# Kernel optimization log

Hardware: AMD Instinct MI355X
Metric: run time of the kernel (lower is better)

Reference implementation:

```python
import jax, jax.numpy as jnp
import numpy as np

N_HEADS = 16
EPS = 1e-4


def setup_inputs() -> dict:
    key = jax.random.key(0)
    ks = jax.random.split(key, 9)
    B, L, E = 4, 4096, 1024
    s = 1.0 / np.sqrt(E)
    return {
        "x": jax.random.normal(ks[0], (B, L, E), dtype=jnp.float32),
        "Wq": jax.random.normal(ks[1], (E, E), dtype=jnp.float32) * s,
        "bq": jax.random.normal(ks[2], (E,), dtype=jnp.float32) * 0.01,
        "Wk": jax.random.normal(ks[3], (E, E), dtype=jnp.float32) * s,
        "bk": jax.random.normal(ks[4], (E,), dtype=jnp.float32) * 0.01,
        "Wv": jax.random.normal(ks[5], (E, E), dtype=jnp.float32) * s,
        "bv": jax.random.normal(ks[6], (E,), dtype=jnp.float32) * 0.01,
        "Wo": jax.random.normal(ks[7], (E, E), dtype=jnp.float32) * s,
        "bo": jax.random.normal(ks[8], (E,), dtype=jnp.float32) * 0.01,
    }


def _cosformer(x, Wq, bq, Wk, bk, Wv, bv, Wo, bo):
    B, L, E = x.shape
    H = N_HEADS
    hd = E // H
    # torch Linear: y = x @ W.T + b; self-attention so q=k=v source is x
    q = jax.nn.relu(jnp.einsum('ble,fe->blf', x, Wq) + bq)
    k = jax.nn.relu(jnp.einsum('ble,fe->blf', x, Wk) + bk)
    v = jnp.einsum('ble,fe->blf', x, Wv) + bv
    # (B, L, E) -> (B*H, L, hd)  [matches torch view(L, B*H, hd).transpose(0,1)]
    def split_heads(t):
        return t.reshape(B, L, H, hd).transpose(0, 2, 1, 3).reshape(B * H, L, hd)
    q, k, v = split_heads(q), split_heads(k), split_heads(v)
    m = L  # src_len == tgt_len
    idx = (np.pi / 2) * jnp.arange(1, m + 1, dtype=jnp.float32) / m  # (m,)
    sin = jnp.sin(idx)[None, :, None]
    cos = jnp.cos(idx)[None, :, None]
    q_ = jnp.concatenate([q * sin, q * cos], axis=-1)  # (BH, L, 2hd)
    k_ = jnp.concatenate([k * sin, k * cos], axis=-1)
    kv = jnp.einsum('nld,nlm->ndm', k_, v)             # (BH, 2hd, hd)
    z = 1.0 / jnp.maximum(jnp.einsum('nld,nd->nl', q_, k_.sum(axis=1)), EPS)
    attn = jnp.einsum('nld,ndm->nlm', q_, kv) * z[:, :, None]  # (BH, L, hd)
    # (B*H, L, hd) -> (B, L, E)
    out = attn.reshape(B, H, L, hd).transpose(0, 2, 1, 3).reshape(B, L, E)
    return jnp.einsum('ble,fe->blf', out, Wo) + bo


def reference(x, Wq, bq, Wk, bk, Wv, bv, Wo, bo):
    return _cosformer(x, Wq, bq, Wk, bk, Wv, bv, Wo, bo)
```

## Files before the change

kernel.cpp:

```cpp
#include <hip/hip_runtime.h>


typedef unsigned short u16;
typedef unsigned int u32;
typedef __attribute__((ext_vector_type(8))) __bf16 bf16x8;
typedef __attribute__((ext_vector_type(4))) float f32x4;

#define PI_HALF 1.57079632679489662f
#define EPS_Z 1e-4f

__device__ __forceinline__ u16 f32_to_bf16(float f) {
    union { float f; unsigned int u; } x; x.f = f;
    unsigned int lsb = (x.u >> 16) & 1u;
    x.u += 0x7fffu + lsb;
    return (u16)(x.u >> 16);
}
__device__ __forceinline__ float bf16_to_f32(u16 u) {
    union { float f; unsigned int u; } x; x.u = ((unsigned int)u) << 16;
    return x.f;
}

typedef __attribute__((address_space(1))) void amdgpu_global_t;
typedef __attribute__((address_space(3))) void amdgpu_lds_t;
__device__ __forceinline__ void async_load16(const u16* g, u16* l) {
    __builtin_amdgcn_global_load_lds((amdgpu_global_t*)g, (amdgpu_lds_t*)l, 16, 0, 0);
}

__global__ __launch_bounds__(256) void cvt_bf16(const float* __restrict__ in,
                                                u16* __restrict__ out, int n4) {
    int i = blockIdx.x * 256 + threadIdx.x;
    if (i >= n4) return;
    float4 f = ((const float4*)in)[i];
    ushort4 o;
    o.x = f32_to_bf16(f.x); o.y = f32_to_bf16(f.y);
    o.z = f32_to_bf16(f.z); o.w = f32_to_bf16(f.w);
    ((ushort4*)out)[i] = o;
}

__global__ __launch_bounds__(256) void cvt_w4(const float* __restrict__ w0,
                                              const float* __restrict__ w1,
                                              const float* __restrict__ w2,
                                              const float* __restrict__ w3,
                                              u16* __restrict__ wcat) {
    const float* src = (blockIdx.y == 0) ? w0 : (blockIdx.y == 1) ? w1
                     : (blockIdx.y == 2) ? w2 : w3;
    u16* dst = wcat + (size_t)blockIdx.y * 1048576;
    int i = blockIdx.x * 256 + threadIdx.x;
    float4 f = ((const float4*)src)[i];
    ushort4 o;
    o.x = f32_to_bf16(f.x); o.y = f32_to_bf16(f.y);
    o.z = f32_to_bf16(f.z); o.w = f32_to_bf16(f.w);
    ((ushort4*)dst)[i] = o;
}

__device__ __forceinline__ void gemm256_core(const u16* __restrict__ Abase,
                                             const u16* __restrict__ Bbase,
                                             u16* As, u16* Bs,
                                             f32x4 (&acc)[8][4]) {
    const int tid  = threadIdx.x;
    const int wave = tid >> 6;
    const int lane = tid & 63;
    const int quad = lane >> 4;
    const int l15  = lane & 15;
    const int wr   = wave >> 2;
    const int wc   = wave & 3;
    const int srow = tid >> 3;
    const int scg  = (tid & 7) ^ (srow & 7);

    const u16* Ag = Abase + ((long)srow << 10) + scg * 8;
    const u16* Bg = Bbase + ((long)srow << 10) + scg * 8;

    auto stage = [&](const u16* g, u16* lb, int hs, int t) {
        async_load16(g + ((long)hs << 16) + (t << 6), lb + hs * 4096);
    };
    auto rdA = [&](const u16* buf, int mf, int kk) -> bf16x8 {
        const int R = wr * 128 + mf * 16 + l15;
        return *(const bf16x8*)(buf + R * 64 + ((kk * 32 + quad * 8) ^ ((R & 7) * 8)));
    };
    auto rdB = [&](const u16* buf, int nf, int kk) -> bf16x8 {
        const int R = wc * 64 + nf * 16 + l15;
        return *(const bf16x8*)(buf + R * 64 + ((kk * 32 + quad * 8) ^ ((R & 7) * 8)));
    };

    bf16x8 a[4][2], b[4][2];
    auto mfma8 = [&](int i0, int j0) {
        __builtin_amdgcn_s_setprio(1);
#pragma unroll
        for (int i = 0; i < 4; ++i)
#pragma unroll
            for (int j = 0; j < 2; ++j)
#pragma unroll
                for (int kk = 0; kk < 2; ++kk)
                    acc[i0 + i][j0 + j] = __builtin_amdgcn_mfma_f32_16x16x32_bf16(
                        a[i][kk], b[j0 + j][kk], acc[i0 + i][j0 + j], 0, 0, 0);
        __builtin_amdgcn_s_setprio(0);
    };

#pragma unroll
    for (int hs = 0; hs < 4; ++hs) stage(Ag, As + wave * 512, hs, 0);
#pragma unroll
    for (int hs = 0; hs < 4; ++hs) stage(Bg, Bs + wave * 512, hs, 0);
#pragma unroll
    for (int hs = 0; hs < 4; ++hs) stage(Ag, As + 16384 + wave * 512, hs, 1);
#pragma unroll
    for (int hs = 0; hs < 4; ++hs) stage(Bg, Bs + 16384 + wave * 512, hs, 1);
    asm volatile("s_waitcnt vmcnt(8)" ::: "memory");
    __builtin_amdgcn_s_barrier();

#pragma unroll 1
    for (int t = 0; t < 16; ++t) {
        const int cur = t & 1;
        const u16* Ab = As + cur * 16384;
        const u16* Bb = Bs + cur * 16384;
        u16* lA = As + cur * 16384 + wave * 512;
        u16* lB = Bs + cur * 16384 + wave * 512;
        const bool pf = (t < 14);

#pragma unroll
        for (int i = 0; i < 4; ++i) { a[i][0] = rdA(Ab, i, 0); a[i][1] = rdA(Ab, i, 1); }
#pragma unroll
        for (int j = 0; j < 2; ++j) { b[j][0] = rdB(Bb, j, 0); b[j][1] = rdB(Bb, j, 1); }
        mfma8(0, 0);
#pragma unroll
        for (int j = 2; j < 4; ++j) { b[j][0] = rdB(Bb, j, 0); b[j][1] = rdB(Bb, j, 1); }
        mfma8(0, 2);
#pragma unroll
        for (int i = 0; i < 4; ++i) { a[i][0] = rdA(Ab, i + 4, 0); a[i][1] = rdA(Ab, i + 4, 1); }
        mfma8(4, 0);

        __builtin_amdgcn_s_barrier();
        asm volatile("" ::: "memory");
        if (pf) {
#pragma unroll
            for (int hs = 0; hs < 4; ++hs) stage(Bg, lB, hs, t + 2);
#pragma unroll
            for (int hs = 0; hs < 4; ++hs) stage(Ag, lA, hs, t + 2);
        }
        mfma8(4, 2);
        if (pf) {
            asm volatile("s_waitcnt vmcnt(8)" ::: "memory");
        } else {
            asm volatile("s_waitcnt vmcnt(0)" ::: "memory");
        }
        __builtin_amdgcn_s_barrier();
        asm volatile("" ::: "memory");
    }
}

__global__ __launch_bounds__(512, 2) void gemm_qkv(const u16* __restrict__ A,
                                                   const u16* __restrict__ Wcat,
                                                   const float* __restrict__ bq,
                                                   const float* __restrict__ bk,
                                                   const float* __restrict__ bv,
                                                   u16* __restrict__ qo,
                                                   u16* __restrict__ ko,
                                                   u16* __restrict__ vo) {
    __shared__ __align__(16) u16 As[32768];
    __shared__ __align__(16) u16 Bs[32768];
    const int bid = blockIdx.x;
    const int swz = (bid & 7) * 96 + (bid >> 3);
    const int bx  = swz / 12;
    const int byy = swz - bx * 12;
    const long tileM = (long)bx * 256;

    f32x4 acc[8][4] = {};
    gemm256_core(A + (tileM << 10), Wcat + ((long)byy << 18), As, Bs, acc);

    const int tid  = (int)threadIdx.x;
    const int wave = tid >> 6;
    const int lane = tid & 63;
    const int quad = lane >> 4, l15 = lane & 15;
    const int wr = wave >> 2, wc = wave & 3;
    const int mat = byy >> 2;
    const float* bias = (mat == 0) ? bq : (mat == 1) ? bk : bv;
    u16* outp = (mat == 0) ? qo : (mat == 1) ? ko : vo;
    const bool relu = (mat < 2);
    const int ncol0 = (byy & 3) * 256;

    const int rloc = tid >> 5;
    const int c8   = (tid & 31) * 8;
#pragma unroll 1
    for (int pass = 0; pass < 2; ++pass) {
        __syncthreads();
        if (wr == pass) {
#pragma unroll
            for (int i = 0; i < 8; ++i)
#pragma unroll
                for (int j = 0; j < 4; ++j) {
                    const int col = wc * 64 + j * 16 + l15;
                    const float bb = bias[ncol0 + col];
#pragma unroll
                    for (int r = 0; r < 4; ++r) {
                        const int row = i * 16 + quad * 4 + r;
                        float v = acc[i][j][r] + bb;
                        if (relu) v = fmaxf(v, 0.0f);
                        As[row * 256 + col] = f32_to_bf16(v);
                    }
                }
        }
        __syncthreads();
        const long gr0 = tileM + pass * 128;
#pragma unroll
        for (int it = 0; it < 8; ++it) {
            const int row = it * 16 + rloc;
            uint4 t4 = *(const uint4*)&As[row * 256 + c8];
            *(uint4*)&outp[(gr0 + row) * 1024 + ncol0 + c8] = t4;
        }
    }
}

__global__ __launch_bounds__(512, 2) void gemm_o(const u16* __restrict__ A,
                                                 const u16* __restrict__ Bw,
                                                 const float* __restrict__ bias,
                                                 float* __restrict__ Cout) {
    __shared__ __align__(16) u16 As[32768];
    __shared__ __align__(16) u16 Bs[32768];
    const int bid = blockIdx.x;
    const int swz = (bid & 7) * 32 + (bid >> 3);
    const long tileM = (long)(swz >> 2) * 256;
    const long tileN = (long)(swz & 3) * 256;

    f32x4 acc[8][4] = {};
    gemm256_core(A + (tileM << 10), Bw + (tileN << 10), As, Bs, acc);

    const int wave = (int)threadIdx.x >> 6;
    const int lane = (int)threadIdx.x & 63;
    const int quad = lane >> 4, l15 = lane & 15;
    const int wr = wave >> 2, wc = wave & 3;
#pragma unroll
    for (int j = 0; j < 4; ++j) {
        const long n = tileN + wc * 64 + j * 16 + l15;
        const float bb = bias[n];
#pragma unroll
        for (int i = 0; i < 8; ++i) {
            const long m0 = tileM + wr * 128 + i * 16 + quad * 4;
#pragma unroll
            for (int r = 0; r < 4; ++r)
                Cout[(m0 + r) * 1024 + n] = acc[i][j][r] + bb;
        }
    }
}

__global__ __launch_bounds__(256) void kv_mfma(const u16* __restrict__ kmat,
                                               const u16* __restrict__ vmat,
                                               float* __restrict__ part) {
    __shared__ u16 Ak[64 * 40];
    __shared__ u16 Bv[64 * 40];
    const int tid = threadIdx.x;
    const int wave = tid >> 6, lane = tid & 63;
    const int quad = lane >> 4, l15 = lane & 15;
    const int head = blockIdx.y;
    const int b = head >> 4, h = head & 15;
    const int l0 = blockIdx.x * 512;
    const int sl = tid >> 3;
    const int sc8 = tid & 7;
    const int scol = sl ^ ((sc8 & 3) << 3);
    const int krow_base = (wave & 1) * 32;
    const bool use_cos = (wave >> 1) != 0;
    const int mbase = wave * 32;

    float sv[8], cv[8];
#pragma unroll
    for (int e = 0; e < 8; e++) {
        float ang = (PI_HALF / 4096.0f) * (float)(l0 + quad * 8 + e + 1);
        sv[e] = sinf(ang); cv[e] = cosf(ang);
    }
    const float cD = 0.9999247018391445f;
    const float sD = 0.0122715382857199f;

    bf16x8 onesf;
#pragma unroll
    for (int e = 0; e < 8; e++)
        onesf[e] = (l15 == 0) ? (__bf16)1.0f : (__bf16)0.0f;

    f32x4 acc[2][5] = {};

    long row = ((long)b * 4096 + l0 + sl) * 1024 + h * 64 + sc8 * 8;
    uint4 kk = *(const uint4*)(kmat + row);
    uint4 vv = *(const uint4*)(vmat + row);

    for (int kt = 0; kt < 16; kt++) {
        uint4 kk_n = {}, vv_n = {};
        if (kt < 15) {
            row += 32 * 1024;
            kk_n = *(const uint4*)(kmat + row);
            vv_n = *(const uint4*)(vmat + row);
        }
        const u16* kp = (const u16*)&kk;
        const u16* vp = (const u16*)&vv;
#pragma unroll
        for (int e = 0; e < 8; e++) {
            const int d = sc8 * 8 + e;
            Ak[d * 40 + scol] = kp[e];
            Bv[d * 40 + scol] = vp[e];
        }
        __syncthreads();

        bf16x8 af[2];
#pragma unroll
        for (int i = 0; i < 2; i++) {
            const int d = krow_base + i * 16 + l15;
            const int q2 = (quad ^ ((d >> 3) & 3)) * 8;
            bf16x8 raw = *(const bf16x8*)&Ak[d * 40 + q2];
            bf16x8 sc;
#pragma unroll
            for (int e = 0; e < 8; e++)
                sc[e] = (__bf16)((float)raw[e] * (use_cos ? cv[e] : sv[e]));
            af[i] = sc;
        }
        bf16x8 bfr[5];
#pragma unroll
        for (int j = 0; j < 4; j++) {
            const int n = j * 16 + l15;
            const int q2 = (quad ^ ((n >> 3) & 3)) * 8;
            bfr[j] = *(const bf16x8*)&Bv[n * 40 + q2];
        }
        bfr[4] = onesf;
#pragma unroll
        for (int i = 0; i < 2; i++)
#pragma unroll
            for (int j = 0; j < 5; j++)
                acc[i][j] = __builtin_amdgcn_mfma_f32_16x16x32_bf16(
                    af[i], bfr[j], acc[i][j], 0, 0, 0);

#pragma unroll
        for (int e = 0; e < 8; e++) {
            const float ns = sv[e] * cD + cv[e] * sD;
            cv[e] = cv[e] * cD - sv[e] * sD;
            sv[e] = ns;
        }
        __syncthreads();
        kk = kk_n; vv = vv_n;
    }

    float* op = part + ((long)blockIdx.x * 64 + head) * 10240;
#pragma unroll
    for (int i = 0; i < 2; i++)
#pragma unroll
        for (int j = 0; j < 5; j++)
#pragma unroll
            for (int r = 0; r < 4; r++)
                op[(mbase + i * 16 + quad * 4 + r) * 80 + j * 16 + l15] = acc[i][j][r];
}

__global__ __launch_bounds__(256) void kv_reduce_t(const float* __restrict__ part,
                                                   u16* __restrict__ Bt) {
    __shared__ float accs[32 * 81];
    const int head = blockIdx.y, d2t = blockIdx.x;
    const float* bp = part + (long)head * 10240 + d2t * 32 * 80;
    for (int idx = threadIdx.x; idx < 2560; idx += 256) {
        float s = 0.0f;
#pragma unroll
        for (int c = 0; c < 8; c++) s += bp[(long)c * 655360 + idx];
        const int d2 = idx / 80, n = idx - d2 * 80;
        accs[d2 * 81 + n] = s;
    }
    __syncthreads();
    for (int idx = threadIdx.x; idx < 2560; idx += 256) {
        const int n = idx >> 5, d2 = idx & 31;
        Bt[(long)head * 10240 + n * 128 + d2t * 32 + d2] = f32_to_bf16(accs[d2 * 81 + n]);
    }
}

__global__ __launch_bounds__(256) void attn_mfma(const u16* __restrict__ qb,
                                                 const u16* __restrict__ Bt,
                                                 u16* __restrict__ merged) {
    __shared__ __align__(16) u16 As[128 * 72];
    __shared__ __align__(16) u16 Bs[80 * 136];
    const int tid = threadIdx.x;
    const int wave = tid >> 6, lane = tid & 63;
    const int quad = lane >> 4, l15 = lane & 15;
    const int head = blockIdx.y;
    const int b = head >> 4, h = head & 15;
    const int tm = blockIdx.x * 128;
    const long b4 = (long)b * 4096;

    for (int c = tid; c < 1024; c += 256) {
        const int row = c >> 3, c8 = c & 7;
        uint4 t = *(const uint4*)(qb + (b4 + tm + row) * 1024 + h * 64 + c8 * 8);
        *(uint4*)&As[row * 72 + c8 * 8] = t;
    }
    for (int c = tid; c < 1280; c += 256) {
        const int row = c >> 4, c16 = c & 15;
        uint4 t = *(const uint4*)(Bt + (long)head * 10240 + row * 128 + c16 * 8);
        *(uint4*)&Bs[row * 136 + c16 * 8] = t;
    }
    const int wm = wave * 32;
    float snl[2], csl[2];
#pragma unroll
    for (int i = 0; i < 2; i++) {
        const int l = tm + wm + i * 16 + l15;
        const float idx = PI_HALF * (float)(l + 1) * (1.0f / 4096.0f);
        snl[i] = sinf(idx); csl[i] = cosf(idx);
    }
    __syncthreads();

    f32x4 acc[2][5] = {};
#pragma unroll
    for (int kb = 0; kb < 4; kb++) {
        const int qc = (kb & 1) * 32 + quad * 8;
        bf16x8 af[2];
#pragma unroll
        for (int i = 0; i < 2; i++) {
            bf16x8 raw = *(const bf16x8*)&As[(wm + i * 16 + l15) * 72 + qc];
            const float s = (kb < 2) ? snl[i] : csl[i];
            bf16x8 sc;
#pragma unroll
            for (int e = 0; e < 8; e++) sc[e] = (__bf16)((float)raw[e] * s);
            af[i] = sc;
        }
        bf16x8 bf[5];
#pragma unroll
        for (int j = 0; j < 5; j++)
            bf[j] = *(const bf16x8*)&Bs[(j * 16 + l15) * 136 + kb * 32 + quad * 8];
#pragma unroll
        for (int i = 0; i < 2; i++)
#pragma unroll
            for (int j = 0; j < 5; j++)
                acc[i][j] = __builtin_amdgcn_mfma_f32_16x16x32_bf16(
                    af[i], bf[j], acc[i][j], 0, 0, 0);
    }

    __syncthreads();
#pragma unroll
    for (int i = 0; i < 2; i++) {
        float z[4];
#pragma unroll
        for (int r = 0; r < 4; r++) {
            const float den = __shfl(acc[i][4][r], lane & 0x30, 64);
            z[r] = 1.0f / fmaxf(den, EPS_Z);
        }
#pragma unroll
        for (int j = 0; j < 4; j++)
#pragma unroll
            for (int r = 0; r < 4; r++) {
                const int row = wm + i * 16 + quad * 4 + r;
                As[row * 64 + j * 16 + l15] = f32_to_bf16(acc[i][j][r] * z[r]);
            }
    }
    __syncthreads();
    const int rloc = tid >> 3, c8 = (tid & 7) * 8;
#pragma unroll
    for (int it = 0; it < 4; ++it) {
        const int row = it * 32 + rloc;
        uint4 t4 = *(const uint4*)&As[row * 64 + c8];
        *(uint4*)&merged[(b4 + tm + row) * 1024 + h * 64 + c8] = t4;
    }
}

extern "C" void kernel_launch(void* const* d_in, const int* in_sizes, int n_in,
                              void* d_out, int out_size, void* d_ws, size_t ws_size,
                              hipStream_t stream) {
    (void)in_sizes; (void)n_in; (void)out_size; (void)ws_size;
    const float* x  = (const float*)d_in[0];
    const float* Wq = (const float*)d_in[1];
    const float* bq = (const float*)d_in[2];
    const float* Wk = (const float*)d_in[3];
    const float* bk = (const float*)d_in[4];
    const float* Wv = (const float*)d_in[5];
    const float* bv = (const float*)d_in[6];
    const float* Wo = (const float*)d_in[7];
    const float* bo = (const float*)d_in[8];
    float* out = (float*)d_out;

    const int M = 16384, E = 1024;
    char* ws = (char*)d_ws;
    const size_t MB = 1048576;
    u16* xb   = (u16*)(ws);
    u16* qb   = (u16*)(ws + 32 * MB);
    u16* kb   = (u16*)(ws + 64 * MB);
    u16* vb   = (u16*)(ws + 96 * MB);
    u16* wcat = (u16*)(ws + 128 * MB);
    u16* wob  = wcat + 3 * (size_t)E * E;
    u16* Btb  = (u16*)(ws + 136 * MB);
    float* part = (float*)xb;
    u16* mergedb = kb;

    cvt_bf16<<<dim3(M * E / 4 / 256), dim3(256), 0, stream>>>(x, xb, M * E / 4);
    cvt_w4<<<dim3(E * E / 4 / 256, 4), dim3(256), 0, stream>>>(Wq, Wk, Wv, Wo, wcat);

    gemm_qkv<<<dim3(768), dim3(512), 0, stream>>>(xb, wcat, bq, bk, bv, qb, kb, vb);

    kv_mfma<<<dim3(8, 64), dim3(256), 0, stream>>>(kb, vb, part);
    kv_reduce_t<<<dim3(4, 64), dim3(256), 0, stream>>>(part, Btb);
    attn_mfma<<<dim3(32, 64), dim3(256), 0, stream>>>(qb, Btb, mergedb);

    gemm_o<<<dim3(256), dim3(512), 0, stream>>>(mergedb, wob, bo, out);
}
```

Measured before the change: 343.9 us.

## Shrink GEMM tiles to 128x256 with BK=32 for higher occupancy

Changes the shared GEMM core from 256x256 tiles with a K-step of 64 to 128x256 tiles with a K-step of 32. Shared memory per block drops from 128KB to 48KB and launch bounds rise to 4 blocks per CU. Both the QKV and output projection grids double to fill the CUs and hide latency. The LDS swizzle and the epilogue staging layout are redone to match. In exchange, each tile reuses its data less, so more global and LDS traffic per FLOP, and the loop runs more barrier iterations.

```diff
diff --git a/kernel.cpp b/kernel.cpp
--- a/kernel.cpp
+++ b/kernel.cpp
@@ -14,10 +14,6 @@
     unsigned int lsb = (x.u >> 16) & 1u;
     x.u += 0x7fffu + lsb;
     return (u16)(x.u >> 16);
-}
-__device__ __forceinline__ float bf16_to_f32(u16 u) {
-    union { float f; unsigned int u; } x; x.u = ((unsigned int)u) << 16;
-    return x.f;
 }
 
 typedef __attribute__((address_space(1))) void amdgpu_global_t;
@@ -53,10 +49,10 @@
     ((ushort4*)dst)[i] = o;
 }
 
-__device__ __forceinline__ void gemm256_core(const u16* __restrict__ Abase,
+__device__ __forceinline__ void gemm128_core(const u16* __restrict__ Abase,
                                              const u16* __restrict__ Bbase,
                                              u16* As, u16* Bs,
-                                             f32x4 (&acc)[8][4]) {
+                                             f32x4 (&acc)[4][4]) {
     const int tid  = threadIdx.x;
     const int wave = tid >> 6;
     const int lane = tid & 63;
@@ -64,81 +60,58 @@
     const int l15  = lane & 15;
     const int wr   = wave >> 2;
     const int wc   = wave & 3;
-    const int srow = tid >> 3;
-    const int scg  = (tid & 7) ^ (srow & 7);
+    const int srow = tid >> 2;
+    const int scg  = (tid & 3) ^ ((srow >> 1) & 3);
+    const int sg   = (quad ^ ((l15 >> 1) & 3)) * 8;
 
     const u16* Ag = Abase + ((long)srow << 10) + scg * 8;
     const u16* Bg = Bbase + ((long)srow << 10) + scg * 8;
 
-    auto stage = [&](const u16* g, u16* lb, int hs, int t) {
-        async_load16(g + ((long)hs << 16) + (t << 6), lb + hs * 4096);
+    auto stage = [&](int cur, int t) {
+        async_load16(Ag + (t << 5),              As + cur * 4096 + tid * 8);
+        async_load16(Bg + (t << 5),              Bs + cur * 8192 + tid * 8);
+        async_load16(Bg + (1 << 17) + (t << 5),  Bs + cur * 8192 + 4096 + tid * 8);
     };
-    auto rdA = [&](const u16* buf, int mf, int kk) -> bf16x8 {
-        const int R = wr * 128 + mf * 16 + l15;
-        return *(const bf16x8*)(buf + R * 64 + ((kk * 32 + quad * 8) ^ ((R & 7) * 8)));
+    auto rdA = [&](int cur, int mf) -> bf16x8 {
+        return *(const bf16x8*)(As + cur * 4096 + (wr * 64 + mf * 16 + l15) * 32 + sg);
     };
-    auto rdB = [&](const u16* buf, int nf, int kk) -> bf16x8 {
-        const int R = wc * 64 + nf * 16 + l15;
-        return *(const bf16x8*)(buf + R * 64 + ((kk * 32 + quad * 8) ^ ((R & 7) * 8)));
+    auto rdB = [&](int cur, int nf) -> bf16x8 {
+        return *(const bf16x8*)(Bs + cur * 8192 + (wc * 64 + nf * 16 + l15) * 32 + sg);
     };
 
-    bf16x8 a[4][2], b[4][2];
-    auto mfma8 = [&](int i0, int j0) {
+    stage(0, 0);
+    stage(1, 1);
+    asm volatile("s_waitcnt vmcnt(3)" ::: "memory");
+    __builtin_amdgcn_s_barrier();
+
+#pragma unroll 1
+    for (int t = 0; t < 32; ++t) {
+        const int cur = t & 1;
+        bf16x8 a[4], b[4];
+#pragma unroll
+        for (int i = 0; i < 4; ++i) a[i] = rdA(cur, i);
+        b[0] = rdB(cur, 0); b[1] = rdB(cur, 1);
         __builtin_amdgcn_s_setprio(1);
 #pragma unroll
-        for (int i = 0; i < 4; ++i)
-#pragma unroll
-            for (int j = 0; j < 2; ++j)
-#pragma unroll
-                for (int kk = 0; kk < 2; ++kk)
-                    acc[i0 + i][j0 + j] = __builtin_amdgcn_mfma_f32_16x16x32_bf16(
-                        a[i][kk], b[j0 + j][kk], acc[i0 + i][j0 + j], 0, 0, 0);
+        for (int i = 0; i < 4; ++i) {
+            acc[i][0] = __builtin_amdgcn_mfma_f32_16x16x32_bf16(a[i], b[0], acc[i][0], 0, 0, 0);
+            acc[i][1] = __builtin_amdgcn_mfma_f32_16x16x32_bf16(a[i], b[1], acc[i][1], 0, 0, 0);
+        }
         __builtin_amdgcn_s_setprio(0);
-    };
-
-#pragma unroll
-    for (int hs = 0; hs < 4; ++hs) stage(Ag, As + wave * 512, hs, 0);
-#pragma unroll
-    for (int hs = 0; hs < 4; ++hs) stage(Bg, Bs + wave * 512, hs, 0);
-#pragma unroll
-    for (int hs = 0; hs < 4; ++hs) stage(Ag, As + 16384 + wave * 512, hs, 1);
-#pragma unroll
-    for (int hs = 0; hs < 4; ++hs) stage(Bg, Bs + 16384 + wave * 512, hs, 1);
-    asm volatile("s_waitcnt vmcnt(8)" ::: "memory");
-    __builtin_amdgcn_s_barrier();
-
-#pragma unroll 1
-    for (int t = 0; t < 16; ++t) {
-        const int cur = t & 1;
-        const u16* Ab = As + cur * 16384;
-        const u16* Bb = Bs + cur * 16384;
-        u16* lA = As + cur * 16384 + wave * 512;
-        u16* lB = Bs + cur * 16384 + wave * 512;
-        const bool pf = (t < 14);
-
-#pragma unroll
-        for (int i = 0; i < 4; ++i) { a[i][0] = rdA(Ab, i, 0); a[i][1] = rdA(Ab, i, 1); }
-#pragma unroll
-        for (int j = 0; j < 2; ++j) { b[j][0] = rdB(Bb, j, 0); b[j][1] = rdB(Bb, j, 1); }
-        mfma8(0, 0);
-#pragma unroll
-        for (int j = 2; j < 4; ++j) { b[j][0] = rdB(Bb, j, 0); b[j][1] = rdB(Bb, j, 1); }
-        mfma8(0, 2);
-#pragma unroll
-        for (int i = 0; i < 4; ++i) { a[i][0] = rdA(Ab, i + 4, 0); a[i][1] = rdA(Ab, i + 4, 1); }
-        mfma8(4, 0);
+        b[2] = rdB(cur, 2); b[3] = rdB(cur, 3);
+        __builtin_amdgcn_s_setprio(1);
+#pragma unroll
+        for (int i = 0; i < 4; ++i) {
+            acc[i][2] = __builtin_amdgcn_mfma_f32_16x16x32_bf16(a[i], b[2], acc[i][2], 0, 0, 0);
+            acc[i][3] = __builtin_amdgcn_mfma_f32_16x16x32_bf16(a[i], b[3], acc[i][3], 0, 0, 0);
+        }
+        __builtin_amdgcn_s_setprio(0);
 
         __builtin_amdgcn_s_barrier();
         asm volatile("" ::: "memory");
-        if (pf) {
-#pragma unroll
-            for (int hs = 0; hs < 4; ++hs) stage(Bg, lB, hs, t + 2);
-#pragma unroll
-            for (int hs = 0; hs < 4; ++hs) stage(Ag, lA, hs, t + 2);
-        }
-        mfma8(4, 2);
-        if (pf) {
-            asm volatile("s_waitcnt vmcnt(8)" ::: "memory");
+        if (t < 30) {
+            stage(cur, t + 2);
+            asm volatile("s_waitcnt vmcnt(3)" ::: "memory");
         } else {
             asm volatile("s_waitcnt vmcnt(0)" ::: "memory");
         }
@@ -147,7 +120,7 @@
     }
 }
 
-__global__ __launch_bounds__(512, 2) void gemm_qkv(const u16* __restrict__ A,
+__global__ __launch_bounds__(512, 4) void gemm_qkv(const u16* __restrict__ A,
                                                    const u16* __restrict__ Wcat,
                                                    const float* __restrict__ bq,
                                                    const float* __restrict__ bk,
@@ -155,16 +128,16 @@
                                                    u16* __restrict__ qo,
                                                    u16* __restrict__ ko,
                                                    u16* __restrict__ vo) {
-    __shared__ __align__(16) u16 As[32768];
-    __shared__ __align__(16) u16 Bs[32768];
+    __shared__ __align__(16) u16 As[8192];
+    __shared__ __align__(16) u16 Bs[16384];
     const int bid = blockIdx.x;
-    const int swz = (bid & 7) * 96 + (bid >> 3);
+    const int swz = (bid & 7) * 192 + (bid >> 3);
     const int bx  = swz / 12;
     const int byy = swz - bx * 12;
-    const long tileM = (long)bx * 256;
-
-    f32x4 acc[8][4] = {};
-    gemm256_core(A + (tileM << 10), Wcat + ((long)byy << 18), As, Bs, acc);
+    const long tileM = (long)bx * 128;
+
+    f32x4 acc[4][4] = {};
+    gemm128_core(A + (tileM << 10), Wcat + ((long)byy << 18), As, Bs, acc);
 
     const int tid  = (int)threadIdx.x;
     const int wave = tid >> 6;
@@ -177,66 +150,69 @@
     const bool relu = (mat < 2);
     const int ncol0 = (byy & 3) * 256;
 
-    const int rloc = tid >> 5;
-    const int c8   = (tid & 31) * 8;
 #pragma unroll 1
     for (int pass = 0; pass < 2; ++pass) {
         __syncthreads();
         if (wr == pass) {
 #pragma unroll
-            for (int i = 0; i < 8; ++i)
-#pragma unroll
-                for (int j = 0; j < 4; ++j) {
-                    const int col = wc * 64 + j * 16 + l15;
+            for (int mf = 0; mf < 4; ++mf)
+#pragma unroll
+                for (int nf = 0; nf < 4; ++nf) {
+                    const int col = wc * 64 + nf * 16 + l15;
                     const float bb = bias[ncol0 + col];
+                    const int gs = ((col >> 3) ^ (quad << 1)) * 8 + (col & 7);
 #pragma unroll
                     for (int r = 0; r < 4; ++r) {
-                        const int row = i * 16 + quad * 4 + r;
-                        float v = acc[i][j][r] + bb;
+                        const int row = mf * 16 + quad * 4 + r;
+                        float v = acc[mf][nf][r] + bb;
                         if (relu) v = fmaxf(v, 0.0f);
-                        As[row * 256 + col] = f32_to_bf16(v);
+                        Bs[row * 256 + gs] = f32_to_bf16(v);
                     }
                 }
         }
         __syncthreads();
-        const long gr0 = tileM + pass * 128;
-#pragma unroll
-        for (int it = 0; it < 8; ++it) {
+        const int rloc = tid >> 5, gg = tid & 31;
+        const long gr0 = tileM + pass * 64;
+#pragma unroll
+        for (int it = 0; it < 4; ++it) {
             const int row = it * 16 + rloc;
-            uint4 t4 = *(const uint4*)&As[row * 256 + c8];
-            *(uint4*)&outp[(gr0 + row) * 1024 + ncol0 + c8] = t4;
-        }
-    }
-}
-
-__global__ __launch_bounds__(512, 2) void gemm_o(const u16* __restrict__ A,
+            const int gsr = gg ^ (((row >> 2) & 3) << 1);
+            uint4 t4 = *(const uint4*)&Bs[row * 256 + gsr * 8];
+            *(uint4*)&outp[(gr0 + row) * 1024 + ncol0 + gg * 8] = t4;
+        }
+    }
+}
+
+__global__ __launch_bounds__(512, 4) void gemm_o(const u16* __restrict__ A,
                                                  const u16* __restrict__ Bw,
                                                  const float* __restrict__ bias,
                                                  float* __restrict__ Cout) {
-    __shared__ __align__(16) u16 As[32768];
-    __shared__ __align__(16) u16 Bs[32768];
+    __shared__ __align__(16) u16 As[8192];
+    __shared__ __align__(16) u16 Bs[16384];
     const int bid = blockIdx.x;
-    const int swz = (bid & 7) * 32 + (bid >> 3);
-    const long tileM = (long)(swz >> 2) * 256;
-    const long tileN = (long)(swz & 3) * 256;
-
-    f32x4 acc[8][4] = {};
-    gemm256_core(A + (tileM << 10), Bw + (tileN << 10), As, Bs, acc);
+    const int swz = (bid & 7) * 64 + (bid >> 3);
+    const int bx  = swz >> 2;
+    const int byy = swz & 3;
+    const long tileM = (long)bx * 128;
+    const long tileN = (long)byy * 256;
+
+    f32x4 acc[4][4] = {};
+    gemm128_core(A + (tileM << 10), Bw + (tileN << 10), As, Bs, acc);
 
     const int wave = (int)threadIdx.x >> 6;
     const int lane = (int)threadIdx.x & 63;
     const int quad = lane >> 4, l15 = lane & 15;
     const int wr = wave >> 2, wc = wave & 3;
 #pragma unroll
-    for (int j = 0; j < 4; ++j) {
-        const long n = tileN + wc * 64 + j * 16 + l15;
+    for (int nf = 0; nf < 4; ++nf) {
+        const long n = tileN + wc * 64 + nf * 16 + l15;
         const float bb = bias[n];
 #pragma unroll
-        for (int i = 0; i < 8; ++i) {
-            const long m0 = tileM + wr * 128 + i * 16 + quad * 4;
+        for (int mf = 0; mf < 4; ++mf) {
+            const long m0 = tileM + wr * 64 + mf * 16 + quad * 4;
 #pragma unroll
             for (int r = 0; r < 4; ++r)
-                Cout[(m0 + r) * 1024 + n] = acc[i][j][r] + bb;
+                Cout[(m0 + r) * 1024 + n] = acc[mf][nf][r] + bb;
         }
     }
 }
@@ -479,11 +455,11 @@
     cvt_bf16<<<dim3(M * E / 4 / 256), dim3(256), 0, stream>>>(x, xb, M * E / 4);
     cvt_w4<<<dim3(E * E / 4 / 256, 4), dim3(256), 0, stream>>>(Wq, Wk, Wv, Wo, wcat);
 
-    gemm_qkv<<<dim3(768), dim3(512), 0, stream>>>(xb, wcat, bq, bk, bv, qb, kb, vb);
+    gemm_qkv<<<dim3(1536), dim3(512), 0, stream>>>(xb, wcat, bq, bk, bv, qb, kb, vb);
 
     kv_mfma<<<dim3(8, 64), dim3(256), 0, stream>>>(kb, vb, part);
     kv_reduce_t<<<dim3(4, 64), dim3(256), 0, stream>>>(part, Btb);
     attn_mfma<<<dim3(32, 64), dim3(256), 0, stream>>>(qb, Btb, mergedb);
 
-    gemm_o<<<dim3(256), dim3(512), 0, stream>>>(mergedb, wob, bo, out);
-}
+    gemm_o<<<dim3(512), dim3(512), 0, stream>>>(mergedb, wob, bo, out);
+}
```

Result: slower. 352.3 us (+2.4%).
